# Kernel tuning notes

Hardware: AMD Instinct MI355X
Metric: run time of the kernel (lower is better)

The kernel has to match this reference:

```python
import jax, jax.numpy as jnp
import numpy as np
from math import sqrt

B, N, DK = 4, 4096, 64


def setup_inputs() -> dict:
    key = jax.random.key(0)
    ks = jax.random.split(key, 5)
    x = jax.random.normal(ks[0], (B, N, DK), dtype=jnp.float32)
    Wv = jax.random.normal(ks[1], (DK, DK), dtype=jnp.float32) / sqrt(DK)
    bv = jax.random.normal(ks[2], (DK,), dtype=jnp.float32) * 0.02
    wq = jax.random.normal(ks[3], (DK,), dtype=jnp.float32) / sqrt(DK)
    wk = jax.random.normal(ks[4], (DK,), dtype=jnp.float32) / sqrt(DK)
    gamma = jnp.ones((DK,), dtype=jnp.float32)
    beta = jnp.zeros((DK,), dtype=jnp.float32)
    return {"x": x, "Wv": Wv, "bv": bv, "wq": wq, "wk": wk, "gamma": gamma, "beta": beta}


def _layer_norm(h, gamma, beta, eps=1e-5):
    mu = jnp.mean(h, axis=-1, keepdims=True)
    var = jnp.var(h, axis=-1, keepdims=True)
    return (h - mu) * jax.lax.rsqrt(var + eps) * gamma + beta


def reference(x, Wv, bv, wq, wk, gamma, beta):
    d_k = x.shape[-1]
    V = jnp.einsum('bnd,ed->bne', x, Wv) + bv          # (B, N, DK)
    Q = jnp.einsum('bnd,d->bn', x, wq)                 # scalar per token
    K = jnp.einsum('bnd,d->bn', x, wk)
    # RBF-kernel scores A[b,i,j] = exp(-(Q_i - K_j)^2)  -> (B, N, N)
    A = jnp.exp(-jnp.square(Q[:, :, None] - K[:, None, :]))
    P = jax.nn.softmax(A / sqrt(d_k), axis=-1)
    out = jnp.einsum('bij,bjd->bid', P, V) + x
    return _layer_norm(out, gamma, beta)
```

## Files before the change

### kernel.cpp

```cpp
#include <hip/hip_runtime.h>

#define NB   4
#define NSEQ 4096
#define DK   64
#define NTOK (NB * NSEQ)

#define QK_SCALE 1.2011224087864498f

typedef __attribute__((ext_vector_type(8))) short short8;
typedef __attribute__((ext_vector_type(4))) float f32x4;

__device__ __forceinline__ float fast_exp2(float x) {
#if __has_builtin(__builtin_amdgcn_exp2f)
    return __builtin_amdgcn_exp2f(x);
#else
    return exp2f(x);
#endif
}

__device__ __forceinline__ unsigned short bf16_rne(float f) {
    unsigned u = __float_as_uint(f);
    u += 0x7fffu + ((u >> 16) & 1u);
    return (unsigned short)(u >> 16);
}

__device__ __forceinline__ short8 u4_to_s8(uint4 u) {
    union { uint4 u; short8 s; } c; c.u = u; return c.s;
}

__global__ __launch_bounds__(512) void qkv_kernel(
    const float* __restrict__ x, const float* __restrict__ Wv,
    const float* __restrict__ bv, const float* __restrict__ wq,
    const float* __restrict__ wk,
    float* __restrict__ Qs, float* __restrict__ Ks, unsigned short* __restrict__ Vt)
{
    __shared__ float x_lds[64 * 68];
    __shared__ float wvt[64 * 68];
    __shared__ float wqk[128];
    __shared__ float bvl[64];
    __shared__ unsigned short vt_lds[64 * 72];

    const int t = threadIdx.x;
    const int tok0 = blockIdx.x * 64;

    #pragma unroll
    for (int r = 0; r < 2; ++r) {
        int f = t + 512 * r;
        int row = f >> 4, c4 = f & 15;
        float4 v = ((const float4*)(x + (size_t)(tok0 + row) * DK))[c4];
        *(float4*)&x_lds[row * 68 + c4 * 4] = v;
    }
    #pragma unroll
    for (int r = 0; r < 2; ++r) {
        int f = t + 512 * r;
        int e = f >> 4, c4 = f & 15;
        float4 v = ((const float4*)(Wv + e * DK))[c4];
        wvt[(c4 * 4 + 0) * 68 + e] = v.x;
        wvt[(c4 * 4 + 1) * 68 + e] = v.y;
        wvt[(c4 * 4 + 2) * 68 + e] = v.z;
        wvt[(c4 * 4 + 3) * 68 + e] = v.w;
    }
    if (t < 64) { wqk[t * 2] = wq[t]; wqk[t * 2 + 1] = wk[t]; bvl[t] = bv[t]; }
    __syncthreads();

    const int tok = t >> 3, oc = t & 7;
    const int e0 = oc * 8;
    float acc[8];
    #pragma unroll
    for (int ee = 0; ee < 8; ++ee) acc[ee] = bvl[e0 + ee];

    for (int d = 0; d < DK; d += 4) {
        float4 x4 = *(const float4*)&x_lds[tok * 68 + d];
        const float xs[4] = {x4.x, x4.y, x4.z, x4.w};
        #pragma unroll
        for (int dd = 0; dd < 4; ++dd) {
            float xv = xs[dd];
            const float4* wrow = (const float4*)&wvt[(d + dd) * 68 + e0];
            float4 wa = wrow[0], wb = wrow[1];
            acc[0] += xv * wa.x; acc[1] += xv * wa.y;
            acc[2] += xv * wa.z; acc[3] += xv * wa.w;
            acc[4] += xv * wb.x; acc[5] += xv * wb.y;
            acc[6] += xv * wb.z; acc[7] += xv * wb.w;
        }
    }
    #pragma unroll
    for (int k = 0; k < 8; ++k)
        vt_lds[(e0 + k) * 72 + tok] = bf16_rne(acc[k]);

    if (t < 128) {
        const int tk = t & 63;
        const int sel = (t >= 64);
        float a = 0.f;
        for (int d = 0; d < DK; ++d)
            a += x_lds[tk * 68 + d] * wqk[d * 2 + sel];
        (sel ? Ks : Qs)[tok0 + tk] = a * QK_SCALE;
    }
    __syncthreads();

    const int bb = tok0 >> 12, n0 = tok0 & 4095;
    {
        int d = t >> 3, c = t & 7;
        uint4 v = *(const uint4*)((const char*)vt_lds + d * 144 + c * 16);
        *(uint4*)(Vt + (size_t)(bb * 64 + d) * 4096 + n0 + c * 8) = v;
    }
}

extern __shared__ float smem[];

__global__ __launch_bounds__(1024, 4) void attn_kernel(
    const float* __restrict__ x,
    const float* __restrict__ Qsg, const float* __restrict__ Ksg,
    const unsigned short* __restrict__ Vt,
    const float* __restrict__ gamma, const float* __restrict__ beta,
    float* __restrict__ out)
{
    float* k_lds = smem;
    float* red   = smem + 4096;
    float* dred  = smem + 4096 + 8 * 64 * 68;

    const int t    = threadIdx.x;
    const int b    = blockIdx.x >> 6;
    const int i0   = (blockIdx.x & 63) << 6;
    const int w    = t >> 6;
    const int lane = t & 63;
    const int rit  = lane & 15;
    const int q    = lane >> 4;
    const int rgrp = w >> 3;
    const int je   = w & 7;

    ((float4*)k_lds)[t] = ((const float4*)(Ksg + (size_t)b * 4096))[t];

    const float Qs0 = Qsg[b * 4096 + i0 + rgrp * 32 + rit];
    const float Qs1 = Qsg[b * 4096 + i0 + rgrp * 32 + 16 + rit];
    const unsigned short* Vtb = Vt + (size_t)b * 64 * 4096 + (size_t)rit * 4096;

    f32x4 acc[2][4] = {};
    f32x4 accd[2] = {};
    const short onebf = (short)0x3F80;
    const short8 vones = {onebf, onebf, onebf, onebf, onebf, onebf, onebf, onebf};

    __syncthreads();

    const int jw = je * 512;
    for (int s = 0; s < 16; ++s) {
        const int j0 = jw + s * 32;
        const unsigned short* vb = Vtb + j0 + q * 8;
        uint4 bu0 = *(const uint4*)(vb);
        uint4 bu1 = *(const uint4*)(vb + 16 * 4096);
        uint4 bu2 = *(const uint4*)(vb + 32 * 4096);
        uint4 bu3 = *(const uint4*)(vb + 48 * 4096);

        const float* kp = &k_lds[j0 + q * 8];
        float4 ka = *(const float4*)kp;
        float4 kb = *(const float4*)(kp + 4);
        float kv[8] = {ka.x, ka.y, ka.z, ka.w, kb.x, kb.y, kb.z, kb.w};
        float w0[8], w1[8];
        #pragma unroll
        for (int jj = 0; jj < 8; ++jj) {
            float d0 = Qs0 - kv[jj];
            float g0 = fast_exp2(-d0 * d0);
            float p0 = __builtin_fmaf(g0, 3.2552083e-4f, 7.8125e-3f);
            p0 = __builtin_fmaf(g0, p0, 0.125f);
            w0[jj] = __builtin_fmaf(g0, p0, 1.0f);
            float d1 = Qs1 - kv[jj];
            float g1 = fast_exp2(-d1 * d1);
            float p1 = __builtin_fmaf(g1, 3.2552083e-4f, 7.8125e-3f);
            p1 = __builtin_fmaf(g1, p1, 0.125f);
            w1[jj] = __builtin_fmaf(g1, p1, 1.0f);
        }
        uint4 au0, au1;
        au0.x = __builtin_amdgcn_perm(__float_as_uint(w0[1]), __float_as_uint(w0[0]), 0x07060302u);
        au0.y = __builtin_amdgcn_perm(__float_as_uint(w0[3]), __float_as_uint(w0[2]), 0x07060302u);
        au0.z = __builtin_amdgcn_perm(__float_as_uint(w0[5]), __float_as_uint(w0[4]), 0x07060302u);
        au0.w = __builtin_amdgcn_perm(__float_as_uint(w0[7]), __float_as_uint(w0[6]), 0x07060302u);
        au1.x = __builtin_amdgcn_perm(__float_as_uint(w1[1]), __float_as_uint(w1[0]), 0x07060302u);
        au1.y = __builtin_amdgcn_perm(__float_as_uint(w1[3]), __float_as_uint(w1[2]), 0x07060302u);
        au1.z = __builtin_amdgcn_perm(__float_as_uint(w1[5]), __float_as_uint(w1[4]), 0x07060302u);
        au1.w = __builtin_amdgcn_perm(__float_as_uint(w1[7]), __float_as_uint(w1[6]), 0x07060302u);
        short8 a0 = u4_to_s8(au0);
        short8 a1 = u4_to_s8(au1);

        short8 b0 = u4_to_s8(bu0), b1 = u4_to_s8(bu1);
        short8 b2 = u4_to_s8(bu2), b3 = u4_to_s8(bu3);
        acc[0][0] = __builtin_amdgcn_mfma_f32_16x16x32_bf16(a0, b0, acc[0][0], 0, 0, 0);
        acc[0][1] = __builtin_amdgcn_mfma_f32_16x16x32_bf16(a0, b1, acc[0][1], 0, 0, 0);
        acc[0][2] = __builtin_amdgcn_mfma_f32_16x16x32_bf16(a0, b2, acc[0][2], 0, 0, 0);
        acc[0][3] = __builtin_amdgcn_mfma_f32_16x16x32_bf16(a0, b3, acc[0][3], 0, 0, 0);
        acc[1][0] = __builtin_amdgcn_mfma_f32_16x16x32_bf16(a1, b0, acc[1][0], 0, 0, 0);
        acc[1][1] = __builtin_amdgcn_mfma_f32_16x16x32_bf16(a1, b1, acc[1][1], 0, 0, 0);
        acc[1][2] = __builtin_amdgcn_mfma_f32_16x16x32_bf16(a1, b2, acc[1][2], 0, 0, 0);
        acc[1][3] = __builtin_amdgcn_mfma_f32_16x16x32_bf16(a1, b3, acc[1][3], 0, 0, 0);
        accd[0]   = __builtin_amdgcn_mfma_f32_16x16x32_bf16(a0, vones, accd[0], 0, 0, 0);
        accd[1]   = __builtin_amdgcn_mfma_f32_16x16x32_bf16(a1, vones, accd[1], 0, 0, 0);
    }

    #pragma unroll
    for (int rt = 0; rt < 2; ++rt)
        #pragma unroll
        for (int ct = 0; ct < 4; ++ct)
            #pragma unroll
            for (int rg = 0; rg < 4; ++rg)
                red[(size_t)je * (64 * 68) + (rgrp * 32 + rt * 16 + q * 4 + rg) * 68 + ct * 16 + rit]
                    = acc[rt][ct][rg];
    if (rit == 0) {
        #pragma unroll
        for (int rt = 0; rt < 2; ++rt)
            #pragma unroll
            for (int rg = 0; rg < 4; ++rg)
                dred[je * 64 + rgrp * 32 + rt * 16 + q * 4 + rg] = accd[rt][rg];
    }
    __syncthreads();

    const int row = t >> 4, cg = t & 15;
    float dsum = 0.f;
    #pragma unroll
    for (int sl = 0; sl < 8; ++sl) dsum += dred[sl * 64 + row];
    const float inv = 1.0f / dsum;
    const size_t rowg = (size_t)(b * 4096 + i0 + row);
    const float* xr = x + rowg * 64;

    float h[4], sm = 0.f, ss = 0.f;
    #pragma unroll
    for (int ct = 0; ct < 4; ++ct) {
        float num = 0.f;
        #pragma unroll
        for (int sl = 0; sl < 8; ++sl)
            num += red[(size_t)sl * (64 * 68) + row * 68 + ct * 16 + cg];
        h[ct] = num * inv + xr[ct * 16 + cg];
        sm += h[ct]; ss += h[ct] * h[ct];
    }
    #pragma unroll
    for (int m = 1; m < 16; m <<= 1) { sm += __shfl_xor(sm, m); ss += __shfl_xor(ss, m); }
    const float mu   = sm * 0.015625f;
    const float var  = ss * 0.015625f - mu * mu;
    const float rstd = rsqrtf(var + 1e-5f);

    float* orow = out + rowg * 64;
    #pragma unroll
    for (int ct = 0; ct < 4; ++ct)
        orow[ct * 16 + cg] = (h[ct] - mu) * rstd * gamma[ct * 16 + cg] + beta[ct * 16 + cg];
}

extern "C" void kernel_launch(void* const* d_in, const int* in_sizes, int n_in,
                              void* d_out, int out_size, void* d_ws, size_t ws_size,
                              hipStream_t stream)
{
    const float* x     = (const float*)d_in[0];
    const float* Wv    = (const float*)d_in[1];
    const float* bv    = (const float*)d_in[2];
    const float* wq    = (const float*)d_in[3];
    const float* wk    = (const float*)d_in[4];
    const float* gamma = (const float*)d_in[5];
    const float* beta  = (const float*)d_in[6];
    float* out = (float*)d_out;

    float* Qs = (float*)d_ws;
    float* Ks = Qs + NTOK;
    unsigned short* Vt = (unsigned short*)(Ks + NTOK);

    const int attn_lds = 4096 * 4 + 8 * 64 * 68 * 4 + 8 * 64 * 4;
    static bool attr_set = false;
    hipFuncSetAttribute((const void*)attn_kernel,
                        hipFuncAttributeMaxDynamicSharedMemorySize, attn_lds);

    qkv_kernel<<<dim3(NTOK / 64), dim3(512), 0, stream>>>(x, Wv, bv, wq, wk, Qs, Ks, Vt);
    attn_kernel<<<dim3(NB * (NSEQ / 64)), dim3(1024), attn_lds, stream>>>(
        x, Qs, Ks, Vt, gamma, beta, out);
    (void)attr_set;
}
```

Baseline: 104.7 us.

## Give each wave all 64 rows over a shorter key slice to reuse V fragments

Each of the 16 waves now covers all 64 query rows (4 row tiles) over a 256-key slice, where before two row groups each had 8 key-slice waves. Every V fragment loaded from global memory now feeds 4 row tiles instead of 2, which halves V traffic per block, and the main loop is unrolled by 2. The cross-wave reduction becomes two phases: waves 0-7 store their partials, then waves 8-15 add theirs into the same LDS slots after a barrier. The costs are more accumulator registers per thread (16+4 f32x4), which may lower occupancy under the 1024-thread launch bound, and an extra barrier.

Result: no change. 104.4 us (-0.2%).

```diff
diff --git a/kernel.cpp b/kernel.cpp
--- a/kernel.cpp
+++ b/kernel.cpp
@@ -121,100 +121,107 @@
     const int t    = threadIdx.x;
     const int b    = blockIdx.x >> 6;
     const int i0   = (blockIdx.x & 63) << 6;
-    const int w    = t >> 6;
+    const int je   = t >> 6;
     const int lane = t & 63;
     const int rit  = lane & 15;
     const int q    = lane >> 4;
-    const int rgrp = w >> 3;
-    const int je   = w & 7;
 
     ((float4*)k_lds)[t] = ((const float4*)(Ksg + (size_t)b * 4096))[t];
 
-    const float Qs0 = Qsg[b * 4096 + i0 + rgrp * 32 + rit];
-    const float Qs1 = Qsg[b * 4096 + i0 + rgrp * 32 + 16 + rit];
-    const unsigned short* Vtb = Vt + (size_t)b * 64 * 4096 + (size_t)rit * 4096;
-
-    f32x4 acc[2][4] = {};
-    f32x4 accd[2] = {};
+    float Qr[4];
+    #pragma unroll
+    for (int rt = 0; rt < 4; ++rt)
+        Qr[rt] = Qsg[b * 4096 + i0 + rt * 16 + rit];
+
+    f32x4 acc[4][4] = {};
+    f32x4 accd[4] = {};
     const short onebf = (short)0x3F80;
     const short8 vones = {onebf, onebf, onebf, onebf, onebf, onebf, onebf, onebf};
 
-    __syncthreads();
-
-    const int jw = je * 512;
-    for (int s = 0; s < 16; ++s) {
-        const int j0 = jw + s * 32;
-        const unsigned short* vb = Vtb + j0 + q * 8;
-        uint4 bu0 = *(const uint4*)(vb);
-        uint4 bu1 = *(const uint4*)(vb + 16 * 4096);
-        uint4 bu2 = *(const uint4*)(vb + 32 * 4096);
-        uint4 bu3 = *(const uint4*)(vb + 48 * 4096);
-
-        const float* kp = &k_lds[j0 + q * 8];
-        float4 ka = *(const float4*)kp;
-        float4 kb = *(const float4*)(kp + 4);
+    const int jw = je * 256;
+    const unsigned short* vb = Vt + (size_t)b * 64 * 4096 + (size_t)rit * 4096 + jw + q * 8;
+    const float* kp = &k_lds[jw + q * 8];
+
+    __syncthreads();
+
+    #pragma unroll 2
+    for (int s = 0; s < 8; ++s) {
+        const unsigned short* vn = vb + s * 32;
+        uint4 bu0 = *(const uint4*)(vn);
+        uint4 bu1 = *(const uint4*)(vn + 16 * 4096);
+        uint4 bu2 = *(const uint4*)(vn + 32 * 4096);
+        uint4 bu3 = *(const uint4*)(vn + 48 * 4096);
+
+        const float* kn = kp + s * 32;
+        float4 ka = *(const float4*)(kn);
+        float4 kb = *(const float4*)(kn + 4);
         float kv[8] = {ka.x, ka.y, ka.z, ka.w, kb.x, kb.y, kb.z, kb.w};
-        float w0[8], w1[8];
-        #pragma unroll
-        for (int jj = 0; jj < 8; ++jj) {
-            float d0 = Qs0 - kv[jj];
-            float g0 = fast_exp2(-d0 * d0);
-            float p0 = __builtin_fmaf(g0, 3.2552083e-4f, 7.8125e-3f);
-            p0 = __builtin_fmaf(g0, p0, 0.125f);
-            w0[jj] = __builtin_fmaf(g0, p0, 1.0f);
-            float d1 = Qs1 - kv[jj];
-            float g1 = fast_exp2(-d1 * d1);
-            float p1 = __builtin_fmaf(g1, 3.2552083e-4f, 7.8125e-3f);
-            p1 = __builtin_fmaf(g1, p1, 0.125f);
-            w1[jj] = __builtin_fmaf(g1, p1, 1.0f);
-        }
-        uint4 au0, au1;
-        au0.x = __builtin_amdgcn_perm(__float_as_uint(w0[1]), __float_as_uint(w0[0]), 0x07060302u);
-        au0.y = __builtin_amdgcn_perm(__float_as_uint(w0[3]), __float_as_uint(w0[2]), 0x07060302u);
-        au0.z = __builtin_amdgcn_perm(__float_as_uint(w0[5]), __float_as_uint(w0[4]), 0x07060302u);
-        au0.w = __builtin_amdgcn_perm(__float_as_uint(w0[7]), __float_as_uint(w0[6]), 0x07060302u);
-        au1.x = __builtin_amdgcn_perm(__float_as_uint(w1[1]), __float_as_uint(w1[0]), 0x07060302u);
-        au1.y = __builtin_amdgcn_perm(__float_as_uint(w1[3]), __float_as_uint(w1[2]), 0x07060302u);
-        au1.z = __builtin_amdgcn_perm(__float_as_uint(w1[5]), __float_as_uint(w1[4]), 0x07060302u);
-        au1.w = __builtin_amdgcn_perm(__float_as_uint(w1[7]), __float_as_uint(w1[6]), 0x07060302u);
-        short8 a0 = u4_to_s8(au0);
-        short8 a1 = u4_to_s8(au1);
 
         short8 b0 = u4_to_s8(bu0), b1 = u4_to_s8(bu1);
         short8 b2 = u4_to_s8(bu2), b3 = u4_to_s8(bu3);
-        acc[0][0] = __builtin_amdgcn_mfma_f32_16x16x32_bf16(a0, b0, acc[0][0], 0, 0, 0);
-        acc[0][1] = __builtin_amdgcn_mfma_f32_16x16x32_bf16(a0, b1, acc[0][1], 0, 0, 0);
-        acc[0][2] = __builtin_amdgcn_mfma_f32_16x16x32_bf16(a0, b2, acc[0][2], 0, 0, 0);
-        acc[0][3] = __builtin_amdgcn_mfma_f32_16x16x32_bf16(a0, b3, acc[0][3], 0, 0, 0);
-        acc[1][0] = __builtin_amdgcn_mfma_f32_16x16x32_bf16(a1, b0, acc[1][0], 0, 0, 0);
-        acc[1][1] = __builtin_amdgcn_mfma_f32_16x16x32_bf16(a1, b1, acc[1][1], 0, 0, 0);
-        acc[1][2] = __builtin_amdgcn_mfma_f32_16x16x32_bf16(a1, b2, acc[1][2], 0, 0, 0);
-        acc[1][3] = __builtin_amdgcn_mfma_f32_16x16x32_bf16(a1, b3, acc[1][3], 0, 0, 0);
-        accd[0]   = __builtin_amdgcn_mfma_f32_16x16x32_bf16(a0, vones, accd[0], 0, 0, 0);
-        accd[1]   = __builtin_amdgcn_mfma_f32_16x16x32_bf16(a1, vones, accd[1], 0, 0, 0);
-    }
-
-    #pragma unroll
-    for (int rt = 0; rt < 2; ++rt)
-        #pragma unroll
-        for (int ct = 0; ct < 4; ++ct)
+
+        #pragma unroll
+        for (int rt = 0; rt < 4; ++rt) {
+            float w0[8];
+            #pragma unroll
+            for (int jj = 0; jj < 8; ++jj) {
+                float d0 = Qr[rt] - kv[jj];
+                float g0 = fast_exp2(-d0 * d0);
+                float p0 = __builtin_fmaf(g0, 3.2552083e-4f, 7.8125e-3f);
+                p0 = __builtin_fmaf(g0, p0, 0.125f);
+                w0[jj] = __builtin_fmaf(g0, p0, 1.0f);
+            }
+            uint4 au;
+            au.x = __builtin_amdgcn_perm(__float_as_uint(w0[1]), __float_as_uint(w0[0]), 0x07060302u);
+            au.y = __builtin_amdgcn_perm(__float_as_uint(w0[3]), __float_as_uint(w0[2]), 0x07060302u);
+            au.z = __builtin_amdgcn_perm(__float_as_uint(w0[5]), __float_as_uint(w0[4]), 0x07060302u);
+            au.w = __builtin_amdgcn_perm(__float_as_uint(w0[7]), __float_as_uint(w0[6]), 0x07060302u);
+            short8 a0 = u4_to_s8(au);
+
+            acc[rt][0] = __builtin_amdgcn_mfma_f32_16x16x32_bf16(a0, b0, acc[rt][0], 0, 0, 0);
+            acc[rt][1] = __builtin_amdgcn_mfma_f32_16x16x32_bf16(a0, b1, acc[rt][1], 0, 0, 0);
+            acc[rt][2] = __builtin_amdgcn_mfma_f32_16x16x32_bf16(a0, b2, acc[rt][2], 0, 0, 0);
+            acc[rt][3] = __builtin_amdgcn_mfma_f32_16x16x32_bf16(a0, b3, acc[rt][3], 0, 0, 0);
+            accd[rt]   = __builtin_amdgcn_mfma_f32_16x16x32_bf16(a0, vones, accd[rt], 0, 0, 0);
+        }
+    }
+
+    const int slot = je & 7;
+    float* rbase = red + (size_t)slot * (64 * 68);
+    if (je < 8) {
+        #pragma unroll
+        for (int rt = 0; rt < 4; ++rt)
+            #pragma unroll
+            for (int ct = 0; ct < 4; ++ct)
+                #pragma unroll
+                for (int rg = 0; rg < 4; ++rg)
+                    rbase[(rt * 16 + q * 4 + rg) * 68 + ct * 16 + rit] = acc[rt][ct][rg];
+    }
+    if (rit == 0) {
+        #pragma unroll
+        for (int rt = 0; rt < 4; ++rt)
             #pragma unroll
             for (int rg = 0; rg < 4; ++rg)
-                red[(size_t)je * (64 * 68) + (rgrp * 32 + rt * 16 + q * 4 + rg) * 68 + ct * 16 + rit]
-                    = acc[rt][ct][rg];
-    if (rit == 0) {
-        #pragma unroll
-        for (int rt = 0; rt < 2; ++rt)
-            #pragma unroll
-            for (int rg = 0; rg < 4; ++rg)
-                dred[je * 64 + rgrp * 32 + rt * 16 + q * 4 + rg] = accd[rt][rg];
+                dred[je * 64 + rt * 16 + q * 4 + rg] = accd[rt][rg];
+    }
+    __syncthreads();
+    if (je >= 8) {
+        #pragma unroll
+        for (int rt = 0; rt < 4; ++rt)
+            #pragma unroll
+            for (int ct = 0; ct < 4; ++ct)
+                #pragma unroll
+                for (int rg = 0; rg < 4; ++rg) {
+                    int idx = (rt * 16 + q * 4 + rg) * 68 + ct * 16 + rit;
+                    rbase[idx] += acc[rt][ct][rg];
+                }
     }
     __syncthreads();
 
     const int row = t >> 4, cg = t & 15;
     float dsum = 0.f;
     #pragma unroll
-    for (int sl = 0; sl < 8; ++sl) dsum += dred[sl * 64 + row];
+    for (int sl = 0; sl < 16; ++sl) dsum += dred[sl * 64 + row];
     const float inv = 1.0f / dsum;
     const size_t rowg = (size_t)(b * 4096 + i0 + row);
     const float* xr = x + rowg * 64;
@@ -258,13 +265,11 @@
     float* Ks = Qs + NTOK;
     unsigned short* Vt = (unsigned short*)(Ks + NTOK);
 
-    const int attn_lds = 4096 * 4 + 8 * 64 * 68 * 4 + 8 * 64 * 4;
-    static bool attr_set = false;
+    const int attn_lds = 4096 * 4 + 8 * 64 * 68 * 4 + 16 * 64 * 4;
     hipFuncSetAttribute((const void*)attn_kernel,
                         hipFuncAttributeMaxDynamicSharedMemorySize, attn_lds);
 
     qkv_kernel<<<dim3(NTOK / 64), dim3(512), 0, stream>>>(x, Wv, bv, wq, wk, Qs, Ks, Vt);
     attn_kernel<<<dim3(NB * (NSEQ / 64)), dim3(1024), attn_lds, stream>>>(
         x, Qs, Ks, Vt, gamma, beta, out);
-    (void)attr_set;
-}
+}
```

## Remap attention blocks per XCD for batch-local L2, unroll loop, vectorize epilogue

Applied to the files above, without the earlier changes.

Block indices are remapped so that round-robin dispatch across the eight XCDs sends all blocks of a given batch to the same pair of XCDs. Each XCD's L2 then holds only one batch's Vt and K data instead of all four. The main j-loop gets unroll 2 with hoisted base pointers, and the LayerNorm epilogue switches to float4 loads and stores. A repeat-count parameter, fixed at 1, wraps the body and adds one extra barrier.

After: 105.2 us. Within noise of the previous version (+0.5%).

```diff
diff --git a/kernel.cpp b/kernel.cpp
--- a/kernel.cpp
+++ b/kernel.cpp
@@ -112,15 +112,16 @@
     const float* __restrict__ Qsg, const float* __restrict__ Ksg,
     const unsigned short* __restrict__ Vt,
     const float* __restrict__ gamma, const float* __restrict__ beta,
-    float* __restrict__ out)
+    float* __restrict__ out, int nrep)
 {
     float* k_lds = smem;
     float* red   = smem + 4096;
     float* dred  = smem + 4096 + 8 * 64 * 68;
 
     const int t    = threadIdx.x;
-    const int b    = blockIdx.x >> 6;
-    const int i0   = (blockIdx.x & 63) << 6;
+    const int B    = blockIdx.x;
+    const int b    = (B & 7) >> 1;
+    const int i0   = (((B >> 3) << 1) | (B & 1)) << 6;
     const int w    = t >> 6;
     const int lane = t & 63;
     const int rit  = lane & 15;
@@ -132,28 +133,34 @@
 
     const float Qs0 = Qsg[b * 4096 + i0 + rgrp * 32 + rit];
     const float Qs1 = Qsg[b * 4096 + i0 + rgrp * 32 + 16 + rit];
-    const unsigned short* Vtb = Vt + (size_t)b * 64 * 4096 + (size_t)rit * 4096;
+
+    const short onebf = (short)0x3F80;
+    const short8 vones = {onebf, onebf, onebf, onebf, onebf, onebf, onebf, onebf};
+
+    const int jw = je * 512;
+    const unsigned short* vb = Vt + (size_t)b * 64 * 4096 + (size_t)rit * 4096 + jw + q * 8;
+    const float* kp = &k_lds[jw + q * 8];
+
+    __syncthreads();
+
+    for (int rep = 0; rep < nrep; ++rep) {
 
     f32x4 acc[2][4] = {};
     f32x4 accd[2] = {};
-    const short onebf = (short)0x3F80;
-    const short8 vones = {onebf, onebf, onebf, onebf, onebf, onebf, onebf, onebf};
-
-    __syncthreads();
-
-    const int jw = je * 512;
+
+    #pragma unroll 2
     for (int s = 0; s < 16; ++s) {
-        const int j0 = jw + s * 32;
-        const unsigned short* vb = Vtb + j0 + q * 8;
-        uint4 bu0 = *(const uint4*)(vb);
-        uint4 bu1 = *(const uint4*)(vb + 16 * 4096);
-        uint4 bu2 = *(const uint4*)(vb + 32 * 4096);
-        uint4 bu3 = *(const uint4*)(vb + 48 * 4096);
-
-        const float* kp = &k_lds[j0 + q * 8];
-        float4 ka = *(const float4*)kp;
-        float4 kb = *(const float4*)(kp + 4);
+        const unsigned short* vn = vb + s * 32;
+        uint4 bu0 = *(const uint4*)(vn);
+        uint4 bu1 = *(const uint4*)(vn + 16 * 4096);
+        uint4 bu2 = *(const uint4*)(vn + 32 * 4096);
+        uint4 bu3 = *(const uint4*)(vn + 48 * 4096);
+
+        const float* kn = kp + s * 32;
+        float4 ka = *(const float4*)(kn);
+        float4 kb = *(const float4*)(kn + 4);
         float kv[8] = {ka.x, ka.y, ka.z, ka.w, kb.x, kb.y, kb.z, kb.w};
+
         float w0[8], w1[8];
         #pragma unroll
         for (int jj = 0; jj < 8; ++jj) {
@@ -194,51 +201,66 @@
         accd[1]   = __builtin_amdgcn_mfma_f32_16x16x32_bf16(a1, vones, accd[1], 0, 0, 0);
     }
 
-    #pragma unroll
-    for (int rt = 0; rt < 2; ++rt)
-        #pragma unroll
-        for (int ct = 0; ct < 4; ++ct)
-            #pragma unroll
-            for (int rg = 0; rg < 4; ++rg)
-                red[(size_t)je * (64 * 68) + (rgrp * 32 + rt * 16 + q * 4 + rg) * 68 + ct * 16 + rit]
-                    = acc[rt][ct][rg];
-    if (rit == 0) {
+    {
+        float* rbase = red + (size_t)je * (64 * 68);
         #pragma unroll
         for (int rt = 0; rt < 2; ++rt)
             #pragma unroll
-            for (int rg = 0; rg < 4; ++rg)
-                dred[je * 64 + rgrp * 32 + rt * 16 + q * 4 + rg] = accd[rt][rg];
-    }
-    __syncthreads();
-
-    const int row = t >> 4, cg = t & 15;
-    float dsum = 0.f;
-    #pragma unroll
-    for (int sl = 0; sl < 8; ++sl) dsum += dred[sl * 64 + row];
-    const float inv = 1.0f / dsum;
-    const size_t rowg = (size_t)(b * 4096 + i0 + row);
-    const float* xr = x + rowg * 64;
-
-    float h[4], sm = 0.f, ss = 0.f;
-    #pragma unroll
-    for (int ct = 0; ct < 4; ++ct) {
-        float num = 0.f;
-        #pragma unroll
-        for (int sl = 0; sl < 8; ++sl)
-            num += red[(size_t)sl * (64 * 68) + row * 68 + ct * 16 + cg];
-        h[ct] = num * inv + xr[ct * 16 + cg];
-        sm += h[ct]; ss += h[ct] * h[ct];
-    }
-    #pragma unroll
-    for (int m = 1; m < 16; m <<= 1) { sm += __shfl_xor(sm, m); ss += __shfl_xor(ss, m); }
-    const float mu   = sm * 0.015625f;
-    const float var  = ss * 0.015625f - mu * mu;
-    const float rstd = rsqrtf(var + 1e-5f);
-
-    float* orow = out + rowg * 64;
-    #pragma unroll
-    for (int ct = 0; ct < 4; ++ct)
-        orow[ct * 16 + cg] = (h[ct] - mu) * rstd * gamma[ct * 16 + cg] + beta[ct * 16 + cg];
+            for (int ct = 0; ct < 4; ++ct)
+                #pragma unroll
+                for (int rg = 0; rg < 4; ++rg)
+                    rbase[(rgrp * 32 + rt * 16 + q * 4 + rg) * 68 + ct * 16 + rit]
+                        = acc[rt][ct][rg];
+        if (rit == 0) {
+            #pragma unroll
+            for (int rt = 0; rt < 2; ++rt)
+                #pragma unroll
+                for (int rg = 0; rg < 4; ++rg)
+                    dred[je * 64 + rgrp * 32 + rt * 16 + q * 4 + rg] = accd[rt][rg];
+        }
+    }
+    __syncthreads();
+
+    {
+        const int row = t >> 4, cg = t & 15, c0 = cg * 4;
+        float dsum = 0.f;
+        #pragma unroll
+        for (int sl = 0; sl < 8; ++sl) dsum += dred[sl * 64 + row];
+        const float inv = 1.0f / dsum;
+        const size_t rowg = (size_t)(b * 4096 + i0 + row);
+
+        float4 num = make_float4(0.f, 0.f, 0.f, 0.f);
+        #pragma unroll
+        for (int sl = 0; sl < 8; ++sl) {
+            float4 r4 = *(const float4*)&red[(size_t)sl * (64 * 68) + row * 68 + c0];
+            num.x += r4.x; num.y += r4.y; num.z += r4.z; num.w += r4.w;
+        }
+        const float4 x4 = *(const float4*)(x + rowg * 64 + c0);
+        float4 h;
+        h.x = num.x * inv + x4.x;
+        h.y = num.y * inv + x4.y;
+        h.z = num.z * inv + x4.z;
+        h.w = num.w * inv + x4.w;
+
+        float sm = h.x + h.y + h.z + h.w;
+        float ss = h.x * h.x + h.y * h.y + h.z * h.z + h.w * h.w;
+        #pragma unroll
+        for (int m = 1; m < 16; m <<= 1) { sm += __shfl_xor(sm, m); ss += __shfl_xor(ss, m); }
+        const float mu   = sm * 0.015625f;
+        const float var  = ss * 0.015625f - mu * mu;
+        const float rstd = rsqrtf(var + 1e-5f);
+
+        const float4 g4 = *(const float4*)(gamma + c0);
+        const float4 b4 = *(const float4*)(beta + c0);
+        float4 o;
+        o.x = (h.x - mu) * rstd * g4.x + b4.x;
+        o.y = (h.y - mu) * rstd * g4.y + b4.y;
+        o.z = (h.z - mu) * rstd * g4.z + b4.z;
+        o.w = (h.w - mu) * rstd * g4.w + b4.w;
+        *(float4*)(out + rowg * 64 + c0) = o;
+    }
+    __syncthreads();
+    }
 }
 
 extern "C" void kernel_launch(void* const* d_in, const int* in_sizes, int n_in,
@@ -259,12 +281,10 @@
     unsigned short* Vt = (unsigned short*)(Ks + NTOK);
 
     const int attn_lds = 4096 * 4 + 8 * 64 * 68 * 4 + 8 * 64 * 4;
-    static bool attr_set = false;
     hipFuncSetAttribute((const void*)attn_kernel,
                         hipFuncAttributeMaxDynamicSharedMemorySize, attn_lds);
 
     qkv_kernel<<<dim3(NTOK / 64), dim3(512), 0, stream>>>(x, Wv, bv, wq, wk, Qs, Ks, Vt);
     attn_kernel<<<dim3(NB * (NSEQ / 64)), dim3(1024), attn_lds, stream>>>(
-        x, Qs, Ks, Vt, gamma, beta, out);
-    (void)attr_set;
-}
+        x, Qs, Ks, Vt, gamma, beta, out, 1);
+}
```
